# Kernel optimization log

Measured on AMD Instinct MI355X. Metric: run time of the kernel, lower is better.

Reference implementation:

```python
import jax, jax.numpy as jnp
import numpy as np

B, S, D = 8, 2048, 1024


def setup_inputs() -> dict:
    key = jax.random.key(0)
    k1, k2, k3, k4 = jax.random.split(key, 4)
    scale = 1.0 / np.sqrt(D)
    x = jax.random.normal(k1, (B, S, D), dtype=jnp.float32)
    Wq = jax.random.normal(k2, (D, D), dtype=jnp.float32) * scale
    Wk = jax.random.normal(k3, (D, D), dtype=jnp.float32) * scale
    Wv = jax.random.normal(k4, (D, D), dtype=jnp.float32) * scale
    return {"x": x, "Wq": Wq, "Wk": Wk, "Wv": Wv}


def reference(x, Wq, Wk, Wv):
    # nn.Linear(d, d, bias=False): y = x @ W.T
    q = jnp.einsum('bsd,ed->bse', x, Wq)
    k = jnp.einsum('bsd,ed->bse', x, Wk)
    v = jnp.einsum('bsd,ed->bse', x, Wv)
    S_len = x.shape[1]
    d_k = k.shape[-1]
    # full score matrix, causal mask (strict upper triangle -> -inf)
    scores = jnp.einsum('bqd,bkd->bqk', q, k)
    causal = jnp.triu(jnp.ones((S_len, S_len), dtype=bool), k=1)
    scores = jnp.where(causal[None, :, :], -jnp.inf, scores)
    attn = jax.nn.softmax(scores / jnp.sqrt(jnp.asarray(d_k, scores.dtype)), axis=-1)
    # dropout p=0.0 (eval) -> identity
    return jnp.einsum('bqk,bkd->bqd', attn, v)
```

## Files before the change

kernel.cpp:

```cpp
#include <hip/hip_runtime.h>


typedef _Float16 v8h __attribute__((ext_vector_type(8)));
typedef _Float16 v4h __attribute__((ext_vector_type(4)));
typedef float    v4f __attribute__((ext_vector_type(4)));

#define BM 256
#define BN 256

__device__ __forceinline__ void async16(const _Float16* g, _Float16* l) {
  __builtin_amdgcn_global_load_lds(
      (__attribute__((address_space(1))) void*)(void*)g,
      (__attribute__((address_space(3))) void*)l, 16, 0, 0);
}

__device__ __forceinline__ void gemm_loop(const _Float16* Ab, int lda,
                                          const _Float16* Bb, int ldb,
                                          int NKT, _Float16* lds,
                                          int w, int lane, int wr, int wc,
                                          int lr, int quad, v4f acc[8][4]) {
  int offA[8], offB[4];
#pragma unroll
  for (int i = 0; i < 8; ++i) {
    const int row = wr + i * 16 + lr;
    offA[i] = row * 32 + ((quad ^ ((row >> 1) & 3)) * 8);
  }
#pragma unroll
  for (int j = 0; j < 4; ++j) {
    const int row = wc + j * 16 + lr;
    offB[j] = 8192 + row * 32 + ((quad ^ ((row >> 1) & 3)) * 8);
  }

  const int u0 = w * 128 + lane;
  const int u1 = u0 + 64;
  const int r0 = u0 >> 2, c0 = (u0 & 3) ^ ((r0 >> 1) & 3);
  const int r1 = u1 >> 2, c1 = (u1 & 3) ^ ((r1 >> 1) & 3);
  const _Float16* pA0 = Ab + (size_t)r0 * lda + c0 * 8;
  const _Float16* pA1 = Ab + (size_t)r1 * lda + c1 * 8;
  const _Float16* pB0 = Bb + (size_t)r0 * ldb + c0 * 8;
  const _Float16* pB1 = Bb + (size_t)r1 * ldb + c1 * 8;
  const int dA0 = (w * 128) * 8;
  const int dA1 = (w * 128 + 64) * 8;

#define STAGE(T)                                                             \
  do {                                                                       \
    _Float16* Ld = lds + ((T) & 3) * 16384;                                  \
    async16(pA0 + (T) * 32, Ld + dA0);                                       \
    async16(pB0 + (T) * 32, Ld + 8192 + dA0);                                \
    async16(pA1 + (T) * 32, Ld + dA1);                                       \
    async16(pB1 + (T) * 32, Ld + 8192 + dA1);                                \
  } while (0)

  STAGE(0);
  STAGE(1);
  STAGE(2);
  asm volatile("s_waitcnt vmcnt(8)" ::: "memory");
  __builtin_amdgcn_s_barrier();

  for (int t = 0; t < NKT; ++t) {
    const _Float16* U = lds + (t & 3) * 16384;
    v8h a[8], b[4];
#pragma unroll
    for (int i = 0; i < 8; ++i) a[i] = *(const v8h*)(U + offA[i]);
#pragma unroll
    for (int j = 0; j < 4; ++j) b[j] = *(const v8h*)(U + offB[j]);
    if (t < NKT - 2) {
      asm volatile("s_waitcnt vmcnt(4)" ::: "memory");
    } else {
      asm volatile("s_waitcnt vmcnt(0)" ::: "memory");
    }
    __builtin_amdgcn_s_barrier();
    if (t + 3 < NKT) STAGE(t + 3);
    __builtin_amdgcn_s_setprio(1);
#pragma unroll
    for (int i = 0; i < 8; ++i)
#pragma unroll
      for (int j = 0; j < 4; ++j)
        acc[i][j] = __builtin_amdgcn_mfma_f32_16x16x32_f16(a[i], b[j],
                                                           acc[i][j], 0, 0, 0);
    __builtin_amdgcn_s_setprio(0);
    __builtin_amdgcn_sched_barrier(0);
  }
#undef STAGE
}

__device__ __forceinline__ void grid_swz(int& bx, int& by) {
  const int gx = gridDim.x;
  const int n = gx * gridDim.y;
  const int f = blockIdx.x + blockIdx.y * gx;
  const int s = (f & 7) * (n >> 3) + (f >> 3);
  bx = s % gx;
  by = s / gx;
}

__global__ __launch_bounds__(256)
void cvt_f16(const float* __restrict__ src, _Float16* __restrict__ dst) {
  const int i = (blockIdx.x * 256 + threadIdx.x) * 8;
  float4 a = *(const float4*)(src + i);
  float4 b = *(const float4*)(src + i + 4);
  v8h o = {(_Float16)a.x, (_Float16)a.y, (_Float16)a.z, (_Float16)a.w,
           (_Float16)b.x, (_Float16)b.y, (_Float16)b.z, (_Float16)b.w};
  *(v8h*)(dst + i) = o;
}

__global__ __launch_bounds__(512, 2)
void proj_gemm(const _Float16* __restrict__ X, const _Float16* __restrict__ W,
               _Float16* __restrict__ Qb, _Float16* __restrict__ Kb,
               _Float16* __restrict__ Vt) {
  __shared__ _Float16 lds[65536];
  const int tid = threadIdx.x;
  int bx, by;
  grid_swz(bx, by);
  const int n0 = bx * BN, m0 = by * BM;
  const int which = n0 >> 10;
  const int nw = n0 & 1023;

  const int lane = tid & 63, w = tid >> 6;
  const int wr = (w >> 2) * 128, wc = (w & 3) * 64;
  const int lr = lane & 15, quad = lane >> 4;

  v4f acc[8][4];
#pragma unroll
  for (int i = 0; i < 8; ++i)
#pragma unroll
    for (int j = 0; j < 4; ++j) acc[i][j] = (v4f){0.f, 0.f, 0.f, 0.f};

  gemm_loop(X + (size_t)m0 * 1024, 1024, W + (size_t)n0 * 1024, 1024,
            32, lds, w, lane, wr, wc, lr, quad, acc);

#pragma unroll
  for (int i = 0; i < 8; ++i) {
    const int r0 = m0 + wr + i * 16 + quad * 4;
#pragma unroll
    for (int j = 0; j < 4; ++j) {
      const int cl = wc + j * 16 + lr;
      if (which < 2) {
        _Float16* dst = (which == 0) ? Qb : Kb;
        const int col = nw + cl;
#pragma unroll
        for (int rg = 0; rg < 4; ++rg)
          dst[(size_t)(r0 + rg) * 1024 + col] = (_Float16)acc[i][j][rg];
      } else {
        const int d = nw + cl;
        const int b = r0 >> 11, s = r0 & 2047;
        v4h o = {(_Float16)acc[i][j][0], (_Float16)acc[i][j][1],
                 (_Float16)acc[i][j][2], (_Float16)acc[i][j][3]};
        *(v4h*)(Vt + (size_t)b * 1024 * 2048 + (size_t)d * 2048 + s) = o;
      }
    }
  }
}

__global__ __launch_bounds__(512, 2)
void scores_gemm(const _Float16* __restrict__ Q, const _Float16* __restrict__ K,
                 _Float16* __restrict__ Sc) {
  __shared__ _Float16 lds[65536];
  const int tid = threadIdx.x;
  int bx, by;
  grid_swz(bx, by);
  const int bz = blockIdx.z;
  const int n0 = bx * BN, m0 = by * BM;
  _Float16* Cb = Sc + (size_t)bz * 2048 * 2048;

  if (bx > by) {
    const _Float16 ninf = (_Float16)(-__builtin_inff());
    v8h mv = {ninf, ninf, ninf, ninf, ninf, ninf, ninf, ninf};
#pragma unroll
    for (int it = 0; it < 16; ++it) {
      int ch = it * 512 + tid;
      int r = ch >> 5, cc = (ch & 31) * 8;
      *(v8h*)(Cb + (size_t)(m0 + r) * 2048 + n0 + cc) = mv;
    }
    return;
  }

  const _Float16* Qz = Q + (size_t)bz * 2048 * 1024;
  const _Float16* Kz = K + (size_t)bz * 2048 * 1024;

  const int lane = tid & 63, w = tid >> 6;
  const int wr = (w >> 2) * 128, wc = (w & 3) * 64;
  const int lr = lane & 15, quad = lane >> 4;

  v4f acc[8][4];
#pragma unroll
  for (int i = 0; i < 8; ++i)
#pragma unroll
    for (int j = 0; j < 4; ++j) acc[i][j] = (v4f){0.f, 0.f, 0.f, 0.f};

  gemm_loop(Qz + (size_t)m0 * 1024, 1024, Kz + (size_t)n0 * 1024, 1024,
            32, lds, w, lane, wr, wc, lr, quad, acc);

  const _Float16 ninf = (_Float16)(-__builtin_inff());
#pragma unroll
  for (int i = 0; i < 8; ++i) {
    const int r0 = m0 + wr + i * 16 + quad * 4;
#pragma unroll
    for (int j = 0; j < 4; ++j) {
      const int cc = n0 + wc + j * 16 + lr;
#pragma unroll
      for (int rg = 0; rg < 4; ++rg) {
        const int rr = r0 + rg;
        Cb[(size_t)rr * 2048 + cc] = (cc > rr) ? ninf : (_Float16)acc[i][j][rg];
      }
    }
  }
}

__global__ __launch_bounds__(256)
void softmax_rows(_Float16* __restrict__ Sc) {
  _Float16* base = Sc + (size_t)blockIdx.x * 2048;
  const int tid = threadIdx.x;
  const int lane = tid & 63, w = tid >> 6;

  v8h pv = *(const v8h*)(base + tid * 8);
  float f[8];
#pragma unroll
  for (int j = 0; j < 8; ++j) f[j] = (float)pv[j];

  float mx = f[0];
#pragma unroll
  for (int j = 1; j < 8; ++j) mx = fmaxf(mx, f[j]);
#pragma unroll
  for (int off = 32; off; off >>= 1) mx = fmaxf(mx, __shfl_xor(mx, off));
  __shared__ float redm[4], reds[4];
  if (lane == 0) redm[w] = mx;
  __syncthreads();
  mx = fmaxf(fmaxf(redm[0], redm[1]), fmaxf(redm[2], redm[3]));

  const float scale = 0.03125f;
  float e[8], s = 0.f;
#pragma unroll
  for (int j = 0; j < 8; ++j) {
    e[j] = __expf((f[j] - mx) * scale);
    s += e[j];
  }
#pragma unroll
  for (int off = 32; off; off >>= 1) s += __shfl_xor(s, off);
  if (lane == 0) reds[w] = s;
  __syncthreads();
  s = reds[0] + reds[1] + reds[2] + reds[3];
  const float inv = 1.0f / s;
#pragma unroll
  for (int j = 0; j < 8; ++j) pv[j] = (_Float16)(e[j] * inv);
  *(v8h*)(base + tid * 8) = pv;
}

__global__ __launch_bounds__(512, 2)
void pv_gemm(const _Float16* __restrict__ P, const _Float16* __restrict__ Vt,
             float* __restrict__ Out) {
  __shared__ _Float16 lds[65536];
  const int tid = threadIdx.x;
  int bx, by;
  grid_swz(bx, by);
  const int bz = blockIdx.z;
  const int n0 = bx * BN, m0 = by * BM;
  const _Float16* Pb = P + (size_t)bz * 2048 * 2048;
  const _Float16* Vb = Vt + (size_t)bz * 1024 * 2048;
  float* Cb = Out + (size_t)bz * 2048 * 1024;

  const int lane = tid & 63, w = tid >> 6;
  const int wr = (w >> 2) * 128, wc = (w & 3) * 64;
  const int lr = lane & 15, quad = lane >> 4;

  v4f acc[8][4];
#pragma unroll
  for (int i = 0; i < 8; ++i)
#pragma unroll
    for (int j = 0; j < 4; ++j) acc[i][j] = (v4f){0.f, 0.f, 0.f, 0.f};

  gemm_loop(Pb + (size_t)m0 * 2048, 2048, Vb + (size_t)n0 * 2048, 2048,
            (by + 1) * 8, lds, w, lane, wr, wc, lr, quad, acc);

#pragma unroll
  for (int i = 0; i < 8; ++i) {
    const int r0 = m0 + wr + i * 16 + quad * 4;
#pragma unroll
    for (int j = 0; j < 4; ++j) {
      const int cc = n0 + wc + j * 16 + lr;
#pragma unroll
      for (int rg = 0; rg < 4; ++rg)
        Cb[(size_t)(r0 + rg) * 1024 + cc] = acc[i][j][rg];
    }
  }
}

extern "C" void kernel_launch(void* const* d_in, const int* in_sizes, int n_in,
                              void* d_out, int out_size, void* d_ws, size_t ws_size,
                              hipStream_t stream) {
  const int B = 8, S = 2048, D = 1024;
  const int M = B * S;
  const float* x  = (const float*)d_in[0];
  const float* Wq = (const float*)d_in[1];
  const float* Wk = (const float*)d_in[2];
  const float* Wv = (const float*)d_in[3];
  float* out = (float*)d_out;

  char* ws = (char*)d_ws;
  _Float16* Qb = (_Float16*)ws;
  _Float16* Kb = (_Float16*)(ws + (size_t)33554432);
  _Float16* Vt = (_Float16*)(ws + (size_t)67108864);
  _Float16* Sc = (_Float16*)(ws + (size_t)100663296);
  _Float16* xh = Sc;
  _Float16* Wh = Sc + (size_t)M * D;

  cvt_f16<<<(M * D) / 2048, 256, 0, stream>>>(x, xh);
  cvt_f16<<<(D * D) / 2048, 256, 0, stream>>>(Wq, Wh);
  cvt_f16<<<(D * D) / 2048, 256, 0, stream>>>(Wk, Wh + (size_t)D * D);
  cvt_f16<<<(D * D) / 2048, 256, 0, stream>>>(Wv, Wh + (size_t)2 * D * D);

  proj_gemm<<<dim3(12, M / BM, 1), 512, 0, stream>>>(xh, Wh, Qb, Kb, Vt);

  scores_gemm<<<dim3(S / BN, S / BM, B), 512, 0, stream>>>(Qb, Kb, Sc);

  softmax_rows<<<B * S, 256, 0, stream>>>(Sc);

  pv_gemm<<<dim3(D / BN, S / BM, B), 512, 0, stream>>>(Sc, Vt, out);
}
```

Baseline: 388.7 us.

## Double-buffer LDS fragments in registers and deepen async prefetch to four stages

The GEMM main loop is unrolled by two and keeps two register sets of A/B fragments. The LDS reads for the next k-slice are issued before the MFMA cluster on the current slice, so LDS latency overlaps with matrix math. Global-to-LDS prefetch now runs four stages ahead, with vmcnt waits adjusted to match. Per-fragment offset arrays are replaced by one base offset plus constant strides. The cost is more VGPRs for the second fragment set, which may reduce occupancy, and the loop now assumes an even tile count.

```diff
diff --git a/kernel.cpp b/kernel.cpp
--- a/kernel.cpp
+++ b/kernel.cpp
@@ -12,6 +12,28 @@
   __builtin_amdgcn_global_load_lds(
       (__attribute__((address_space(1))) void*)(void*)g,
       (__attribute__((address_space(3))) void*)l, 16, 0, 0);
+}
+
+__device__ __forceinline__ void read_frags(const _Float16* lds, int slot,
+                                           int offA0, int offB0,
+                                           v8h a[8], v8h b[4]) {
+  const _Float16* base = lds + slot * 16384;
+#pragma unroll
+  for (int i = 0; i < 8; ++i) a[i] = *(const v8h*)(base + offA0 + i * 512);
+#pragma unroll
+  for (int j = 0; j < 4; ++j) b[j] = *(const v8h*)(base + offB0 + j * 512);
+}
+
+__device__ __forceinline__ void mfma_cluster(const v8h a[8], const v8h b[4],
+                                             v4f acc[8][4]) {
+  __builtin_amdgcn_s_setprio(1);
+#pragma unroll
+  for (int i = 0; i < 8; ++i)
+#pragma unroll
+    for (int j = 0; j < 4; ++j)
+      acc[i][j] = __builtin_amdgcn_mfma_f32_16x16x32_f16(a[i], b[j],
+                                                         acc[i][j], 0, 0, 0);
+  __builtin_amdgcn_s_setprio(0);
 }
 
 __device__ __forceinline__ void gemm_loop(const _Float16* Ab, int lda,
@@ -19,17 +41,8 @@
                                           int NKT, _Float16* lds,
                                           int w, int lane, int wr, int wc,
                                           int lr, int quad, v4f acc[8][4]) {
-  int offA[8], offB[4];
-#pragma unroll
-  for (int i = 0; i < 8; ++i) {
-    const int row = wr + i * 16 + lr;
-    offA[i] = row * 32 + ((quad ^ ((row >> 1) & 3)) * 8);
-  }
-#pragma unroll
-  for (int j = 0; j < 4; ++j) {
-    const int row = wc + j * 16 + lr;
-    offB[j] = 8192 + row * 32 + ((quad ^ ((row >> 1) & 3)) * 8);
-  }
+  const int offA0 = (wr + lr) * 32 + ((quad ^ (((wr + lr) >> 1) & 3)) * 8);
+  const int offB0 = 8192 + (wc + lr) * 32 + ((quad ^ (((wc + lr) >> 1) & 3)) * 8);
 
   const int u0 = w * 128 + lane;
   const int u1 = u0 + 64;
@@ -51,37 +64,42 @@
     async16(pB1 + (T) * 32, Ld + 8192 + dA1);                                \
   } while (0)
 
+#define SYNC(T)                                                              \
+  do {                                                                       \
+    asm volatile("s_waitcnt lgkmcnt(0)" ::: "memory");                       \
+    __builtin_amdgcn_sched_barrier(0);                                       \
+    if ((T) <= NKT - 4)                                                      \
+      asm volatile("s_waitcnt vmcnt(8)" ::: "memory");                       \
+    else if ((T) == NKT - 3)                                                 \
+      asm volatile("s_waitcnt vmcnt(4)" ::: "memory");                       \
+    else                                                                     \
+      asm volatile("s_waitcnt vmcnt(0)" ::: "memory");                       \
+    __builtin_amdgcn_s_barrier();                                            \
+  } while (0)
+
+  v8h a0[8], b0[4], a1[8], b1[4];
+
   STAGE(0);
   STAGE(1);
   STAGE(2);
-  asm volatile("s_waitcnt vmcnt(8)" ::: "memory");
+  STAGE(3);
+  asm volatile("s_waitcnt vmcnt(12)" ::: "memory");
   __builtin_amdgcn_s_barrier();
-
-  for (int t = 0; t < NKT; ++t) {
-    const _Float16* U = lds + (t & 3) * 16384;
-    v8h a[8], b[4];
-#pragma unroll
-    for (int i = 0; i < 8; ++i) a[i] = *(const v8h*)(U + offA[i]);
-#pragma unroll
-    for (int j = 0; j < 4; ++j) b[j] = *(const v8h*)(U + offB[j]);
-    if (t < NKT - 2) {
-      asm volatile("s_waitcnt vmcnt(4)" ::: "memory");
-    } else {
-      asm volatile("s_waitcnt vmcnt(0)" ::: "memory");
-    }
-    __builtin_amdgcn_s_barrier();
-    if (t + 3 < NKT) STAGE(t + 3);
-    __builtin_amdgcn_s_setprio(1);
-#pragma unroll
-    for (int i = 0; i < 8; ++i)
-#pragma unroll
-      for (int j = 0; j < 4; ++j)
-        acc[i][j] = __builtin_amdgcn_mfma_f32_16x16x32_f16(a[i], b[j],
-                                                           acc[i][j], 0, 0, 0);
-    __builtin_amdgcn_s_setprio(0);
-    __builtin_amdgcn_sched_barrier(0);
+  read_frags(lds, 0, offA0, offB0, a0, b0);
+
+  for (int t = 0; t < NKT; t += 2) {
+    SYNC(t);
+    if (t + 4 < NKT) STAGE(t + 4);
+    read_frags(lds, (t + 1) & 3, offA0, offB0, a1, b1);
+    mfma_cluster(a0, b0, acc);
+
+    SYNC(t + 1);
+    if (t + 5 < NKT) STAGE(t + 5);
+    if (t + 2 < NKT) read_frags(lds, (t + 2) & 3, offA0, offB0, a0, b0);
+    mfma_cluster(a1, b1, acc);
   }
 #undef STAGE
+#undef SYNC
 }
 
 __device__ __forceinline__ void grid_swz(int& bx, int& by) {
```

After: 403.6 us. +3.9%, slower.

## Software-pipeline LDS fragment reads in GEMM loop and skip masked score tiles

Applied to the files above, without the earlier changes.

The shared GEMM main loop now splits each K-step into two half-tile MFMA groups. A and B fragment reads for the next half are issued from LDS while the current half's MFMAs run, using explicit lgkmcnt waits and an unrolled prologue and epilogue. Separately, the scores kernel no longer writes -inf for fully masked upper tiles, and the softmax only loads and stores columns up to the row's diagonal tile. Together these aim to hide LDS latency behind matrix math and cut memory traffic on the masked region. The cost is fragile hand-written wait counts and more barriers per K-step. Correctness also depends on the PV GEMM never reading the now-uninitialized upper score tiles.

```diff
diff --git a/kernel.cpp b/kernel.cpp
--- a/kernel.cpp
+++ b/kernel.cpp
@@ -13,23 +13,50 @@
       (__attribute__((address_space(1))) void*)(void*)g,
       (__attribute__((address_space(3))) void*)l, 16, 0, 0);
 }
+
+__device__ __forceinline__ void rd_a(const _Float16* U, int offA0, int base,
+                                     v8h a[4]) {
+#pragma unroll
+  for (int i = 0; i < 4; ++i) a[i] = *(const v8h*)(U + offA0 + (base + i) * 512);
+}
+__device__ __forceinline__ void rd_b(const _Float16* U, int offB0, v8h b[4]) {
+#pragma unroll
+  for (int j = 0; j < 4; ++j) b[j] = *(const v8h*)(U + offB0 + j * 512);
+}
+
+__device__ __forceinline__ void mfma16(const v8h a[4], const v8h b[4],
+                                       v4f (*accr)[4]) {
+  __builtin_amdgcn_s_setprio(1);
+#pragma unroll
+  for (int i = 0; i < 4; ++i)
+#pragma unroll
+    for (int j = 0; j < 4; ++j)
+      accr[i][j] = __builtin_amdgcn_mfma_f32_16x16x32_f16(a[i], b[j],
+                                                          accr[i][j], 0, 0, 0);
+  __builtin_amdgcn_s_setprio(0);
+}
+
+#define VM8 asm volatile("s_waitcnt vmcnt(8)" ::: "memory")
+#define VM4 asm volatile("s_waitcnt vmcnt(4)" ::: "memory")
+#define VM0 asm volatile("s_waitcnt vmcnt(0)" ::: "memory")
+#define LG8                                                                  \
+  asm volatile("s_waitcnt lgkmcnt(8)" ::: "memory");                         \
+  __builtin_amdgcn_sched_barrier(0)
+#define LG4                                                                  \
+  asm volatile("s_waitcnt lgkmcnt(4)" ::: "memory");                         \
+  __builtin_amdgcn_sched_barrier(0)
+#define LG0                                                                  \
+  asm volatile("s_waitcnt lgkmcnt(0)" ::: "memory");                         \
+  __builtin_amdgcn_sched_barrier(0)
+#define BAR __builtin_amdgcn_s_barrier()
 
 __device__ __forceinline__ void gemm_loop(const _Float16* Ab, int lda,
                                           const _Float16* Bb, int ldb,
                                           int NKT, _Float16* lds,
                                           int w, int lane, int wr, int wc,
                                           int lr, int quad, v4f acc[8][4]) {
-  int offA[8], offB[4];
-#pragma unroll
-  for (int i = 0; i < 8; ++i) {
-    const int row = wr + i * 16 + lr;
-    offA[i] = row * 32 + ((quad ^ ((row >> 1) & 3)) * 8);
-  }
-#pragma unroll
-  for (int j = 0; j < 4; ++j) {
-    const int row = wc + j * 16 + lr;
-    offB[j] = 8192 + row * 32 + ((quad ^ ((row >> 1) & 3)) * 8);
-  }
+  const int offA0 = (wr + lr) * 32 + ((quad ^ (((wr + lr) >> 1) & 3)) * 8);
+  const int offB0 = 8192 + (wc + lr) * 32 + ((quad ^ (((wc + lr) >> 1) & 3)) * 8);
 
   const int u0 = w * 128 + lane;
   const int u1 = u0 + 64;
@@ -50,38 +77,66 @@
     async16(pA1 + (T) * 32, Ld + dA1);                                       \
     async16(pB1 + (T) * 32, Ld + 8192 + dA1);                                \
   } while (0)
+#define SL(T) (lds + ((T) & 3) * 16384)
+
+  v8h aLo[4], aHi[4], bE[4], bO[4];
 
   STAGE(0);
   STAGE(1);
   STAGE(2);
-  asm volatile("s_waitcnt vmcnt(8)" ::: "memory");
-  __builtin_amdgcn_s_barrier();
-
-  for (int t = 0; t < NKT; ++t) {
-    const _Float16* U = lds + (t & 3) * 16384;
-    v8h a[8], b[4];
-#pragma unroll
-    for (int i = 0; i < 8; ++i) a[i] = *(const v8h*)(U + offA[i]);
-#pragma unroll
-    for (int j = 0; j < 4; ++j) b[j] = *(const v8h*)(U + offB[j]);
-    if (t < NKT - 2) {
-      asm volatile("s_waitcnt vmcnt(4)" ::: "memory");
-    } else {
-      asm volatile("s_waitcnt vmcnt(0)" ::: "memory");
-    }
-    __builtin_amdgcn_s_barrier();
-    if (t + 3 < NKT) STAGE(t + 3);
-    __builtin_amdgcn_s_setprio(1);
-#pragma unroll
-    for (int i = 0; i < 8; ++i)
-#pragma unroll
-      for (int j = 0; j < 4; ++j)
-        acc[i][j] = __builtin_amdgcn_mfma_f32_16x16x32_f16(a[i], b[j],
-                                                           acc[i][j], 0, 0, 0);
-    __builtin_amdgcn_s_setprio(0);
-    __builtin_amdgcn_sched_barrier(0);
-  }
+  VM8;
+  BAR;
+  rd_a(SL(0), offA0, 0, aLo);
+  rd_b(SL(0), offB0, bE);
+
+  for (int t2 = 0; t2 < NKT - 4; t2 += 2) {
+    VM8; BAR;
+    rd_a(SL(t2), offA0, 4, aHi);
+    STAGE(t2 + 3);
+    LG4; mfma16(aLo, bE, &acc[0]);
+    VM8; BAR;
+    rd_a(SL(t2 + 1), offA0, 0, aLo);
+    rd_b(SL(t2 + 1), offB0, bO);
+    LG8; mfma16(aHi, bE, &acc[4]);
+    VM8; BAR;
+    rd_a(SL(t2 + 1), offA0, 4, aHi);
+    STAGE(t2 + 4);
+    LG4; mfma16(aLo, bO, &acc[0]);
+    VM8; BAR;
+    rd_a(SL(t2 + 2), offA0, 0, aLo);
+    rd_b(SL(t2 + 2), offB0, bE);
+    LG8; mfma16(aHi, bO, &acc[4]);
+  }
+
+  VM8; BAR;
+  rd_a(SL(NKT - 4), offA0, 4, aHi);
+  STAGE(NKT - 1);
+  LG4; mfma16(aLo, bE, &acc[0]);
+  VM8; BAR;
+  rd_a(SL(NKT - 3), offA0, 0, aLo);
+  rd_b(SL(NKT - 3), offB0, bO);
+  LG8; mfma16(aHi, bE, &acc[4]);
+  VM8; BAR;
+  rd_a(SL(NKT - 3), offA0, 4, aHi);
+  LG4; mfma16(aLo, bO, &acc[0]);
+  VM4; BAR;
+  rd_a(SL(NKT - 2), offA0, 0, aLo);
+  rd_b(SL(NKT - 2), offB0, bE);
+  LG8; mfma16(aHi, bO, &acc[4]);
+
+  VM4; BAR;
+  rd_a(SL(NKT - 2), offA0, 4, aHi);
+  LG4; mfma16(aLo, bE, &acc[0]);
+  VM0; BAR;
+  rd_a(SL(NKT - 1), offA0, 0, aLo);
+  rd_b(SL(NKT - 1), offB0, bO);
+  LG8; mfma16(aHi, bE, &acc[4]);
+  BAR;
+  rd_a(SL(NKT - 1), offA0, 4, aHi);
+  LG4; mfma16(aLo, bO, &acc[0]);
+  LG0; mfma16(aHi, bO, &acc[4]);
 #undef STAGE
+#undef SL
 }
 
 __device__ __forceinline__ void grid_swz(int& bx, int& by) {
@@ -162,17 +217,7 @@
   const int n0 = bx * BN, m0 = by * BM;
   _Float16* Cb = Sc + (size_t)bz * 2048 * 2048;
 
-  if (bx > by) {
-    const _Float16 ninf = (_Float16)(-__builtin_inff());
-    v8h mv = {ninf, ninf, ninf, ninf, ninf, ninf, ninf, ninf};
-#pragma unroll
-    for (int it = 0; it < 16; ++it) {
-      int ch = it * 512 + tid;
-      int r = ch >> 5, cc = (ch & 31) * 8;
-      *(v8h*)(Cb + (size_t)(m0 + r) * 2048 + n0 + cc) = mv;
-    }
-    return;
-  }
+  if (bx > by) return;
 
   const _Float16* Qz = Q + (size_t)bz * 2048 * 1024;
   const _Float16* Kz = K + (size_t)bz * 2048 * 1024;
@@ -209,13 +254,21 @@
 __global__ __launch_bounds__(256)
 void softmax_rows(_Float16* __restrict__ Sc) {
   _Float16* base = Sc + (size_t)blockIdx.x * 2048;
+  const int q = blockIdx.x & 2047;
+  const int ktile = ((q >> 8) + 1) << 8;
   const int tid = threadIdx.x;
   const int lane = tid & 63, w = tid >> 6;
-
-  v8h pv = *(const v8h*)(base + tid * 8);
+  const bool active = tid * 8 < ktile;
+
   float f[8];
-#pragma unroll
-  for (int j = 0; j < 8; ++j) f[j] = (float)pv[j];
+  if (active) {
+    v8h pv = *(const v8h*)(base + tid * 8);
+#pragma unroll
+    for (int j = 0; j < 8; ++j) f[j] = (float)pv[j];
+  } else {
+#pragma unroll
+    for (int j = 0; j < 8; ++j) f[j] = -__builtin_inff();
+  }
 
   float mx = f[0];
 #pragma unroll
@@ -240,9 +293,12 @@
   __syncthreads();
   s = reds[0] + reds[1] + reds[2] + reds[3];
   const float inv = 1.0f / s;
-#pragma unroll
-  for (int j = 0; j < 8; ++j) pv[j] = (_Float16)(e[j] * inv);
-  *(v8h*)(base + tid * 8) = pv;
+  if (active) {
+    v8h pv;
+#pragma unroll
+    for (int j = 0; j < 8; ++j) pv[j] = (_Float16)(e[j] * inv);
+    *(v8h*)(base + tid * 8) = pv;
+  }
 }
 
 __global__ __launch_bounds__(512, 2)
```

Measured after the change: 397.1 us. 1.02x slower.
